# Kernel optimization log

Measured on AMD Instinct MI355X. Metric: run time of the kernel, lower is better.

## Reference

```python
import jax, jax.numpy as jnp
import numpy as np

N = 100000   # nodes
E = 1600000  # edges (avg degree 16)
D = 128      # in_features == out_features (required by residual branch)


def setup_inputs() -> dict:
    key = jax.random.key(0)
    ks = jax.random.split(key, 8)
    return {
        "x": jax.random.normal(ks[0], (N, D), dtype=jnp.float32),
        "W": jax.random.normal(ks[1], (D, D), dtype=jnp.float32) * (1.0 / np.sqrt(D)),
        "b": jax.random.normal(ks[2], (D,), dtype=jnp.float32) * 0.01,
        "Wres": jax.random.normal(ks[3], (D, D), dtype=jnp.float32) * (1.0 / np.sqrt(D)),
        "bres": jax.random.normal(ks[4], (D,), dtype=jnp.float32) * 0.01,
        "edge_val": jax.random.uniform(ks[5], (E,), dtype=jnp.float32),
        "edge_row": jax.random.randint(ks[6], (E,), 0, N, dtype=jnp.int32),
        "edge_col": jax.random.randint(ks[7], (E,), 0, N, dtype=jnp.int32),
    }


def reference(x, W, b, Wres, bres, edge_val, edge_row, edge_col):
    # Dense projection: [N, D]
    h = x @ W + b
    # Sparse adjacency SpMM: out[i] = sum_{e: row[e]==i} val[e] * h[col[e]]
    msgs = edge_val[:, None] * h[edge_col]            # [E, D] gather
    agg = jax.ops.segment_sum(msgs, edge_row, num_segments=N)  # [N, D] scatter-add
    # Activation (relu), then residual Linear applied to post-activation tensor
    # (faithful to the torch code: x = act(x); x = x + residual(x)).
    a = jax.nn.relu(agg)
    out = a + (a @ Wres + bres)
    # dropout = 0.0 -> identity (eval mode)
    return out
```

## Files before the change

### kernel.cpp

```cpp
#include <hip/hip_runtime.h>
#include <hip/hip_bf16.h>

#define D 128
#define RCH 128
#define NCH 782
#define NCHP 1024
#define NB_S 256
#define CH_S 6250
#define OS2 800
#define CAP 3072
#define GB 1563
#define PB 128

typedef __attribute__((ext_vector_type(8))) short short8v;
typedef __attribute__((ext_vector_type(4))) float float4v;

__device__ inline ushort f2bf(float f) {
    __hip_bfloat16 h = __float2bfloat16(f);
    return __builtin_bit_cast(ushort, h);
}
__device__ inline float bf2f(ushort u) {
    return __builtin_bit_cast(float, (uint)u << 16);
}
__device__ inline ushort relu_bf(ushort u) { return (u & 0x8000u) ? (ushort)0 : u; }

__device__ inline void stage_wt_lds(char* smem, const ushort* __restrict__ Wt,
                                    int tid) {
#pragma unroll
    for (int i = 0; i < 8; ++i) {
        const int L = tid * 128 + i * 16;
        const int row = L >> 8;
        const int off = L & 255;
        *(short8v*)(smem + row * 256 + (off ^ ((row & 7) << 4))) =
            *(const short8v*)((const char*)Wt + L);
    }
}

__global__ __launch_bounds__(256) void k1_prep(const float* __restrict__ W,
                                               const float* __restrict__ Wres,
                                               ushort* __restrict__ Wt,
                                               ushort* __restrict__ Wtres) {
    const int flat = blockIdx.x * 256 + threadIdx.x;
    const float* src = (flat < 16384) ? W : Wres;
    ushort* dst = (flat < 16384) ? Wt : Wtres;
    const int f = flat & 16383;
    const int k = f >> 7, c = f & 127;
    dst[c * D + k] = f2bf(src[f]);
}

__global__ __launch_bounds__(256) void k3_gemm0_p3(const float* __restrict__ X,
                                                   const ushort* __restrict__ Wt,
                                                   const float* __restrict__ bias,
                                                   ushort* __restrict__ hb, int N,
                                                   const float* __restrict__ ev,
                                                   const int* __restrict__ er,
                                                   const int* __restrict__ ec,
                                                   int* __restrict__ offs2,
                                                   int2* __restrict__ tmp, int E) {
    __shared__ char smem[32768];

    if (blockIdx.x < NB_S) {
        int* h = (int*)smem;
        int* sscan = (int*)(smem + 4 * NCHP);
        const int b = blockIdx.x;
        const int t = threadIdx.x;
        const int start = b * CH_S, end = min(E, start + CH_S);

        for (int k = t; k < NCHP; k += 256) h[k] = 0;
        __syncthreads();

        for (int e = start + t; e < end; e += 256)
            atomicAdd(&h[er[e] >> 7], 1);
        __syncthreads();

        const int a0 = h[4 * t], a1 = h[4 * t + 1];
        const int a2 = h[4 * t + 2], a3 = h[4 * t + 3];
        const int tsum = a0 + a1 + a2 + a3;
        sscan[t] = tsum;
        __syncthreads();
        for (int o = 1; o < 256; o <<= 1) {
            const int a = (t >= o) ? sscan[t - o] : 0;
            __syncthreads();
            sscan[t] += a;
            __syncthreads();
        }
        const int ex = b * CH_S + sscan[t] - tsum;
        const int c0 = 4 * t;
        h[c0]     = ex;
        h[c0 + 1] = ex + a0;
        h[c0 + 2] = ex + a0 + a1;
        h[c0 + 3] = ex + a0 + a1 + a2;
        int* od = offs2 + (long)b * OS2;
#pragma unroll
        for (int i = 0; i < 4; ++i)
            if (c0 + i <= NCH) od[c0 + i] = h[c0 + i];
        __syncthreads();

        for (int e = start + t; e < end; e += 256) {
            const int r = er[e];
            const int pos = atomicAdd(&h[r >> 7], 1);
            tmp[pos] = make_int2((ec[e] << 7) | (r & 127), __float_as_int(ev[e]));
        }
        return;
    }

    const int lane = threadIdx.x & 63;
    const int w = threadIdx.x >> 6;
    const int l16 = lane & 15;
    const int lk = lane >> 4;
    const long wRow = (long)(blockIdx.x - NB_S) * 64 + w * 16;

    short8v afrag[4];
    {
        long r = wRow + l16;
        if (r >= N) r = N - 1;
        const float* xp = X + r * D + lk * 8;
#pragma unroll
        for (int ks = 0; ks < 4; ++ks) {
            const float4 u0 = *(const float4*)(xp + ks * 32);
            const float4 u1 = *(const float4*)(xp + ks * 32 + 4);
            float f[8] = {u0.x, u0.y, u0.z, u0.w, u1.x, u1.y, u1.z, u1.w};
            short8v a;
#pragma unroll
            for (int i = 0; i < 8; ++i) a[i] = (short)f2bf(f[i]);
            afrag[ks] = a;
        }
    }

    stage_wt_lds(smem, Wt, threadIdx.x);
    __syncthreads();

    float4v acc[8];
#pragma unroll
    for (int t = 0; t < 8; ++t) acc[t] = (float4v)(0.0f);

    const int swz = (l16 & 7) << 4;
#pragma unroll
    for (int ks = 0; ks < 4; ++ks) {
#pragma unroll
        for (int t = 0; t < 8; ++t) {
            const int row = t * 16 + l16;
            const short8v bfrag = *(const short8v*)(
                smem + row * 256 + ((ks * 64 + lk * 16) ^ swz));
            acc[t] = __builtin_amdgcn_mfma_f32_16x16x32_bf16(afrag[ks], bfrag,
                                                             acc[t], 0, 0, 0);
        }
    }

#pragma unroll
    for (int t = 0; t < 8; ++t) {
        const int col = t * 16 + l16;
        const float bb = bias[col];
#pragma unroll
        for (int i = 0; i < 4; ++i) {
            const long row = wRow + lk * 4 + i;
            if (row < N) hb[row * D + col] = f2bf(acc[t][i] + bb);
        }
    }
}

__global__ __launch_bounds__(256) void k4_sort(const int2* __restrict__ tmp,
                                               const int* __restrict__ offs2,
                                               int2* __restrict__ recs,
                                               int* __restrict__ rowptr) {
    __shared__ int2 buf[CAP];
    __shared__ int sb[256];
    __shared__ int hcnt[RCH];
    __shared__ int sc[RCH];
    __shared__ int cur[RCH];
    const int c = blockIdx.x;
    const int t = threadIdx.x;
    const int s = c * CAP;

    const long ob = (long)t * OS2 + c;
    const int segs = offs2[ob];
    const int sege = offs2[ob + 1];
    const int cb = sege - segs;

    sb[t] = cb;
    __syncthreads();
    for (int o = 1; o < 256; o <<= 1) {
        const int a = (t >= o) ? sb[t - o] : 0;
        __syncthreads();
        sb[t] += a;
        __syncthreads();
    }
    const int base = sb[t] - cb;
    const int cnt = min(sb[255], CAP);

    if (t < RCH) hcnt[t] = 0;
    __syncthreads();

    for (int i = 0; i < cb; ++i) {
        const int p = base + i;
        if (p >= CAP) break;
        const int2 r = tmp[segs + i];
        buf[p] = r;
        atomicAdd(&hcnt[r.x & 127], 1);
    }
    __syncthreads();

    if (t < RCH) sc[t] = hcnt[t];
    __syncthreads();
    for (int o = 1; o < RCH; o <<= 1) {
        const int a = (t < RCH && t >= o) ? sc[t - o] : 0;
        __syncthreads();
        if (t < RCH) sc[t] += a;
        __syncthreads();
    }
    if (t < RCH) {
        const int ex = s + sc[t] - hcnt[t];
        cur[t] = ex;
        rowptr[c * (RCH + 1) + t] = ex;
    }
    if (t == 0) rowptr[c * (RCH + 1) + RCH] = s + cnt;
    __syncthreads();

    for (int k = t; k < cnt; k += 256) {
        const int2 r = buf[k];
        const int pos = atomicAdd(&cur[r.x & 127], 1);
        recs[pos] = make_int2((r.x >> 7) << 8, r.y);
    }
}

#define GFMA2(accv, rr, gg)                                                   \
    accv.x = fmaf(__int_as_float((rr).y), bf2f((ushort)((gg)&0xffffu)), accv.x);\
    accv.y = fmaf(__int_as_float((rr).y), bf2f((ushort)((gg) >> 16)), accv.y);

__device__ inline void drain_row(const int2* __restrict__ recs,
                                 const char* __restrict__ hpc,
                                 int& j, int e, float2& acc) {
    for (; j + 8 <= e; j += 8) {
        const int2 r0 = recs[j],     r1 = recs[j + 1];
        const int2 r2 = recs[j + 2], r3 = recs[j + 3];
        const int2 r4 = recs[j + 4], r5 = recs[j + 5];
        const int2 r6 = recs[j + 6], r7 = recs[j + 7];
        const uint g0 = *(const uint*)(hpc + (uint)r0.x);
        const uint g1 = *(const uint*)(hpc + (uint)r1.x);
        const uint g2 = *(const uint*)(hpc + (uint)r2.x);
        const uint g3 = *(const uint*)(hpc + (uint)r3.x);
        const uint g4 = *(const uint*)(hpc + (uint)r4.x);
        const uint g5 = *(const uint*)(hpc + (uint)r5.x);
        const uint g6 = *(const uint*)(hpc + (uint)r6.x);
        const uint g7 = *(const uint*)(hpc + (uint)r7.x);
        GFMA2(acc, r0, g0) GFMA2(acc, r1, g1) GFMA2(acc, r2, g2) GFMA2(acc, r3, g3)
        GFMA2(acc, r4, g4) GFMA2(acc, r5, g5) GFMA2(acc, r6, g6) GFMA2(acc, r7, g7)
    }
    for (; j + 2 <= e; j += 2) {
        const int2 r0 = recs[j], r1 = recs[j + 1];
        const uint g0 = *(const uint*)(hpc + (uint)r0.x);
        const uint g1 = *(const uint*)(hpc + (uint)r1.x);
        GFMA2(acc, r0, g0) GFMA2(acc, r1, g1)
    }
    if (j < e) {
        const int2 r0 = recs[j];
        const uint g0 = *(const uint*)(hpc + (uint)r0.x);
        GFMA2(acc, r0, g0)
    }
}

__global__ __launch_bounds__(256) void k5_spmm(const ushort* __restrict__ hb,
                                               const int2* __restrict__ recs,
                                               const int* __restrict__ rowptr,
                                               ushort* __restrict__ aggb, int N) {
    const int pair = blockIdx.x * 4 + (threadIdx.x >> 6);
    const int lane = threadIdx.x & 63;
    const int rowA = pair * 2;
    if (rowA >= N) return;

    const int c = rowA >> 7;
    const int tr = rowA & 127;
    int rp = 0;
    if (lane < 3) rp = rowptr[c * (RCH + 1) + tr + lane];
    const int sA = __shfl(rp, 0);
    const int eA = __shfl(rp, 1);
    const int sB = eA;
    const int eB = __shfl(rp, 2);

    const char* hpc = (const char*)hb + lane * 4;
    float2 accA = make_float2(0.f, 0.f);
    float2 accB = make_float2(0.f, 0.f);

    int jA = sA, jB = sB;
    while (jA + 8 <= eA && jB + 8 <= eB) {
        const int2 a0 = recs[jA],     a1 = recs[jA + 1];
        const int2 a2 = recs[jA + 2], a3 = recs[jA + 3];
        const int2 a4 = recs[jA + 4], a5 = recs[jA + 5];
        const int2 a6 = recs[jA + 6], a7 = recs[jA + 7];
        const int2 b0 = recs[jB],     b1 = recs[jB + 1];
        const int2 b2 = recs[jB + 2], b3 = recs[jB + 3];
        const int2 b4 = recs[jB + 4], b5 = recs[jB + 5];
        const int2 b6 = recs[jB + 6], b7 = recs[jB + 7];
        const uint ga0 = *(const uint*)(hpc + (uint)a0.x);
        const uint ga1 = *(const uint*)(hpc + (uint)a1.x);
        const uint ga2 = *(const uint*)(hpc + (uint)a2.x);
        const uint ga3 = *(const uint*)(hpc + (uint)a3.x);
        const uint ga4 = *(const uint*)(hpc + (uint)a4.x);
        const uint ga5 = *(const uint*)(hpc + (uint)a5.x);
        const uint ga6 = *(const uint*)(hpc + (uint)a6.x);
        const uint ga7 = *(const uint*)(hpc + (uint)a7.x);
        const uint gb0 = *(const uint*)(hpc + (uint)b0.x);
        const uint gb1 = *(const uint*)(hpc + (uint)b1.x);
        const uint gb2 = *(const uint*)(hpc + (uint)b2.x);
        const uint gb3 = *(const uint*)(hpc + (uint)b3.x);
        const uint gb4 = *(const uint*)(hpc + (uint)b4.x);
        const uint gb5 = *(const uint*)(hpc + (uint)b5.x);
        const uint gb6 = *(const uint*)(hpc + (uint)b6.x);
        const uint gb7 = *(const uint*)(hpc + (uint)b7.x);
        GFMA2(accA, a0, ga0) GFMA2(accA, a1, ga1) GFMA2(accA, a2, ga2) GFMA2(accA, a3, ga3)
        GFMA2(accA, a4, ga4) GFMA2(accA, a5, ga5) GFMA2(accA, a6, ga6) GFMA2(accA, a7, ga7)
        GFMA2(accB, b0, gb0) GFMA2(accB, b1, gb1) GFMA2(accB, b2, gb2) GFMA2(accB, b3, gb3)
        GFMA2(accB, b4, gb4) GFMA2(accB, b5, gb5) GFMA2(accB, b6, gb6) GFMA2(accB, b7, gb7)
        jA += 8;
        jB += 8;
    }
    drain_row(recs, hpc, jA, eA, accA);
    drain_row(recs, hpc, jB, eB, accB);

    const uint pA = (uint)f2bf(accA.x) | ((uint)f2bf(accA.y) << 16);
    *(uint*)(aggb + (long)rowA * D + lane * 2) = pA;
    const uint pB = (uint)f2bf(accB.x) | ((uint)f2bf(accB.y) << 16);
    *(uint*)(aggb + (long)(rowA + 1) * D + lane * 2) = pB;
}

__global__ __launch_bounds__(256) void k6_gemm1(const ushort* __restrict__ Xb,
                                                const ushort* __restrict__ Wt,
                                                const float* __restrict__ bias,
                                                float* __restrict__ Y, int N) {
    __shared__ char smem[32768];
    const int lane = threadIdx.x & 63;
    const int w = threadIdx.x >> 6;
    const int l16 = lane & 15;
    const int lk = lane >> 4;
    const long wRow = (long)blockIdx.x * 64 + w * 16;

    short8v afrag[4];
    {
        long r = wRow + l16;
        if (r >= N) r = N - 1;
        const ushort* xp = Xb + r * D + lk * 8;
#pragma unroll
        for (int ks = 0; ks < 4; ++ks) {
            short8v a = *(const short8v*)(xp + ks * 32);
#pragma unroll
            for (int i = 0; i < 8; ++i) a[i] = (short)relu_bf((ushort)a[i]);
            afrag[ks] = a;
        }
    }

    stage_wt_lds(smem, Wt, threadIdx.x);
    __syncthreads();

    float4v acc[8];
#pragma unroll
    for (int t = 0; t < 8; ++t) acc[t] = (float4v)(0.0f);

    const int swz = (l16 & 7) << 4;
#pragma unroll
    for (int ks = 0; ks < 4; ++ks) {
#pragma unroll
        for (int t = 0; t < 8; ++t) {
            const int row = t * 16 + l16;
            const short8v bfrag = *(const short8v*)(
                smem + row * 256 + ((ks * 64 + lk * 16) ^ swz));
            acc[t] = __builtin_amdgcn_mfma_f32_16x16x32_bf16(afrag[ks], bfrag,
                                                             acc[t], 0, 0, 0);
        }
    }

#pragma unroll
    for (int t = 0; t < 8; ++t) {
        const int col = t * 16 + l16;
        const float bb = bias[col];
#pragma unroll
        for (int i = 0; i < 4; ++i) {
            const long row = wRow + lk * 4 + i;
            if (row < N) {
                const float a = bf2f(relu_bf(Xb[row * D + col]));
                Y[row * D + col] = a + acc[t][i] + bb;
            }
        }
    }
}

extern "C" void kernel_launch(void* const* d_in, const int* in_sizes, int n_in,
                              void* d_out, int out_size, void* d_ws, size_t ws_size,
                              hipStream_t stream) {
    const float* x    = (const float*)d_in[0];
    const float* W    = (const float*)d_in[1];
    const float* b    = (const float*)d_in[2];
    const float* Wres = (const float*)d_in[3];
    const float* bres = (const float*)d_in[4];
    const float* ev   = (const float*)d_in[5];
    const int*   er   = (const int*)d_in[6];
    const int*   ec   = (const int*)d_in[7];

    float* out = (float*)d_out;

    const int n = in_sizes[0] / D;
    const int e = in_sizes[5];

    char* ws = (char*)d_ws;
    size_t off_b = 0;
    auto alloc = [&](size_t bytes) {
        void* p = ws + off_b;
        off_b += (bytes + 511) & ~size_t(511);
        return p;
    };
    ushort* hb     = (ushort*)alloc((size_t)n * D * sizeof(ushort));
    int2*   recs   = (int2*)alloc((size_t)NCH * CAP * sizeof(int2));
    int*    rowptr = (int*)alloc((size_t)NCH * (RCH + 1) * sizeof(int));
    ushort* Wt     = (ushort*)alloc((size_t)D * D * sizeof(ushort));
    ushort* Wtres  = (ushort*)alloc((size_t)D * D * sizeof(ushort));
    const size_t overlay = off_b;
    int2*   tmp    = (int2*)alloc((size_t)NB_S * CH_S * sizeof(int2));
    int*    offs2  = (int*)alloc((size_t)NB_S * OS2 * sizeof(int));
    size_t aggb_end = overlay + (size_t)n * D * sizeof(ushort);
    if (aggb_end > off_b) off_b = aggb_end;
    ushort* aggb = (ushort*)(ws + overlay);
    (void)ws_size;

    k1_prep<<<PB, 256, 0, stream>>>(W, Wres, Wt, Wtres);

    k3_gemm0_p3<<<NB_S + GB, 256, 0, stream>>>(x, Wt, b, hb, n,
                                               ev, er, ec, offs2, tmp, e);

    k4_sort<<<NCH, 256, 0, stream>>>(tmp, offs2, recs, rowptr);

    k5_spmm<<<(n / 2 + 3) / 4, 256, 0, stream>>>(hb, recs, rowptr, aggb, n);

    k6_gemm1<<<(n + 63) / 64, 256, 0, stream>>>(aggb, Wtres, bres, out, n);
}
```

Before: 162.1 us.

## Split scatter and GEMM into separate kernels with more scatter blocks

Separates the fused edge-bucketing and first-GEMM kernel into two launches. The scatter kernel now uses 500 blocks of 3200 edges, reads edge arrays with int4/float4 vector loads, and the sort kernel has each thread merge two segments. The GEMM kernel processes 128 rows per block, so each staged weight tile is reused twice. This aims to balance the long scatter blocks against GEMM blocks and cut per-edge load overhead, at the cost of an extra launch and losing overlap between the two phases.

Result: no change. 162.4 us (+0.2%).

```diff
diff --git a/kernel.cpp b/kernel.cpp
--- a/kernel.cpp
+++ b/kernel.cpp
@@ -5,11 +5,10 @@
 #define RCH 128
 #define NCH 782
 #define NCHP 1024
-#define NB_S 256
-#define CH_S 6250
+#define NB_S 500
+#define CH_S 3200
 #define OS2 800
 #define CAP 3072
-#define GB 1563
 #define PB 128
 
 typedef __attribute__((ext_vector_type(8))) short short8v;
@@ -48,113 +47,138 @@
     dst[c * D + k] = f2bf(src[f]);
 }
 
-__global__ __launch_bounds__(256) void k3_gemm0_p3(const float* __restrict__ X,
-                                                   const ushort* __restrict__ Wt,
-                                                   const float* __restrict__ bias,
-                                                   ushort* __restrict__ hb, int N,
-                                                   const float* __restrict__ ev,
+__global__ __launch_bounds__(256) void k3a_scatter(const float* __restrict__ ev,
                                                    const int* __restrict__ er,
                                                    const int* __restrict__ ec,
                                                    int* __restrict__ offs2,
                                                    int2* __restrict__ tmp, int E) {
+    __shared__ int h[NCHP];
+    __shared__ int sscan[256];
+    const int b = blockIdx.x;
+    const int t = threadIdx.x;
+    const int start = b * CH_S;
+    const int end = min(E, start + CH_S);
+    const int nfull = (end - start) & ~3;
+
+    for (int k = t; k < NCHP; k += 256) h[k] = 0;
+    __syncthreads();
+
+    for (int o = 4 * t; o < nfull; o += 1024) {
+        const int4 r4 = *(const int4*)(er + start + o);
+        atomicAdd(&h[r4.x >> 7], 1);
+        atomicAdd(&h[r4.y >> 7], 1);
+        atomicAdd(&h[r4.z >> 7], 1);
+        atomicAdd(&h[r4.w >> 7], 1);
+    }
+    for (int o = nfull + t; o < end - start; o += 256)
+        atomicAdd(&h[er[start + o] >> 7], 1);
+    __syncthreads();
+
+    const int a0 = h[4 * t], a1 = h[4 * t + 1];
+    const int a2 = h[4 * t + 2], a3 = h[4 * t + 3];
+    const int tsum = a0 + a1 + a2 + a3;
+    sscan[t] = tsum;
+    __syncthreads();
+    for (int o = 1; o < 256; o <<= 1) {
+        const int a = (t >= o) ? sscan[t - o] : 0;
+        __syncthreads();
+        sscan[t] += a;
+        __syncthreads();
+    }
+    const int ex = start + sscan[t] - tsum;
+    const int c0 = 4 * t;
+    h[c0]     = ex;
+    h[c0 + 1] = ex + a0;
+    h[c0 + 2] = ex + a0 + a1;
+    h[c0 + 3] = ex + a0 + a1 + a2;
+    int* od = offs2 + (long)b * OS2;
+#pragma unroll
+    for (int i = 0; i < 4; ++i)
+        if (c0 + i <= NCH) od[c0 + i] = h[c0 + i];
+    __syncthreads();
+
+    for (int o = 4 * t; o < nfull; o += 1024) {
+        const int4 r4 = *(const int4*)(er + start + o);
+        const int4 c4 = *(const int4*)(ec + start + o);
+        const float4 v4 = *(const float4*)(ev + start + o);
+        const int p0 = atomicAdd(&h[r4.x >> 7], 1);
+        const int p1 = atomicAdd(&h[r4.y >> 7], 1);
+        const int p2 = atomicAdd(&h[r4.z >> 7], 1);
+        const int p3 = atomicAdd(&h[r4.w >> 7], 1);
+        tmp[p0] = make_int2((c4.x << 7) | (r4.x & 127), __float_as_int(v4.x));
+        tmp[p1] = make_int2((c4.y << 7) | (r4.y & 127), __float_as_int(v4.y));
+        tmp[p2] = make_int2((c4.z << 7) | (r4.z & 127), __float_as_int(v4.z));
+        tmp[p3] = make_int2((c4.w << 7) | (r4.w & 127), __float_as_int(v4.w));
+    }
+    for (int o = nfull + t; o < end - start; o += 256) {
+        const int e = start + o;
+        const int r = er[e];
+        const int pos = atomicAdd(&h[r >> 7], 1);
+        tmp[pos] = make_int2((ec[e] << 7) | (r & 127), __float_as_int(ev[e]));
+    }
+}
+
+__global__ __launch_bounds__(256) void k3b_gemm0(const float* __restrict__ X,
+                                                 const ushort* __restrict__ Wt,
+                                                 const float* __restrict__ bias,
+                                                 ushort* __restrict__ hb, int N) {
     __shared__ char smem[32768];
-
-    if (blockIdx.x < NB_S) {
-        int* h = (int*)smem;
-        int* sscan = (int*)(smem + 4 * NCHP);
-        const int b = blockIdx.x;
-        const int t = threadIdx.x;
-        const int start = b * CH_S, end = min(E, start + CH_S);
-
-        for (int k = t; k < NCHP; k += 256) h[k] = 0;
-        __syncthreads();
-
-        for (int e = start + t; e < end; e += 256)
-            atomicAdd(&h[er[e] >> 7], 1);
-        __syncthreads();
-
-        const int a0 = h[4 * t], a1 = h[4 * t + 1];
-        const int a2 = h[4 * t + 2], a3 = h[4 * t + 3];
-        const int tsum = a0 + a1 + a2 + a3;
-        sscan[t] = tsum;
-        __syncthreads();
-        for (int o = 1; o < 256; o <<= 1) {
-            const int a = (t >= o) ? sscan[t - o] : 0;
-            __syncthreads();
-            sscan[t] += a;
-            __syncthreads();
-        }
-        const int ex = b * CH_S + sscan[t] - tsum;
-        const int c0 = 4 * t;
-        h[c0]     = ex;
-        h[c0 + 1] = ex + a0;
-        h[c0 + 2] = ex + a0 + a1;
-        h[c0 + 3] = ex + a0 + a1 + a2;
-        int* od = offs2 + (long)b * OS2;
-#pragma unroll
-        for (int i = 0; i < 4; ++i)
-            if (c0 + i <= NCH) od[c0 + i] = h[c0 + i];
-        __syncthreads();
-
-        for (int e = start + t; e < end; e += 256) {
-            const int r = er[e];
-            const int pos = atomicAdd(&h[r >> 7], 1);
-            tmp[pos] = make_int2((ec[e] << 7) | (r & 127), __float_as_int(ev[e]));
-        }
-        return;
-    }
-
     const int lane = threadIdx.x & 63;
     const int w = threadIdx.x >> 6;
     const int l16 = lane & 15;
     const int lk = lane >> 4;
-    const long wRow = (long)(blockIdx.x - NB_S) * 64 + w * 16;
-
-    short8v afrag[4];
-    {
-        long r = wRow + l16;
-        if (r >= N) r = N - 1;
-        const float* xp = X + r * D + lk * 8;
+
+    stage_wt_lds(smem, Wt, threadIdx.x);
+    __syncthreads();
+
+    const int swz = (l16 & 7) << 4;
+
+#pragma unroll
+    for (int j = 0; j < 2; ++j) {
+        const long wRow = (long)blockIdx.x * 128 + j * 64 + w * 16;
+
+        short8v afrag[4];
+        {
+            long r = wRow + l16;
+            if (r >= N) r = N - 1;
+            const float* xp = X + r * D + lk * 8;
+#pragma unroll
+            for (int ks = 0; ks < 4; ++ks) {
+                const float4 u0 = *(const float4*)(xp + ks * 32);
+                const float4 u1 = *(const float4*)(xp + ks * 32 + 4);
+                float f[8] = {u0.x, u0.y, u0.z, u0.w, u1.x, u1.y, u1.z, u1.w};
+                short8v a;
+#pragma unroll
+                for (int i = 0; i < 8; ++i) a[i] = (short)f2bf(f[i]);
+                afrag[ks] = a;
+            }
+        }
+
+        float4v acc[8];
+#pragma unroll
+        for (int t = 0; t < 8; ++t) acc[t] = (float4v)(0.0f);
+
 #pragma unroll
         for (int ks = 0; ks < 4; ++ks) {
-            const float4 u0 = *(const float4*)(xp + ks * 32);
-            const float4 u1 = *(const float4*)(xp + ks * 32 + 4);
-            float f[8] = {u0.x, u0.y, u0.z, u0.w, u1.x, u1.y, u1.z, u1.w};
-            short8v a;
-#pragma unroll
-            for (int i = 0; i < 8; ++i) a[i] = (short)f2bf(f[i]);
-            afrag[ks] = a;
-        }
-    }
-
-    stage_wt_lds(smem, Wt, threadIdx.x);
-    __syncthreads();
-
-    float4v acc[8];
-#pragma unroll
-    for (int t = 0; t < 8; ++t) acc[t] = (float4v)(0.0f);
-
-    const int swz = (l16 & 7) << 4;
-#pragma unroll
-    for (int ks = 0; ks < 4; ++ks) {
+#pragma unroll
+            for (int t = 0; t < 8; ++t) {
+                const int row = t * 16 + l16;
+                const short8v bfrag = *(const short8v*)(
+                    smem + row * 256 + ((ks * 64 + lk * 16) ^ swz));
+                acc[t] = __builtin_amdgcn_mfma_f32_16x16x32_bf16(afrag[ks], bfrag,
+                                                                 acc[t], 0, 0, 0);
+            }
+        }
+
 #pragma unroll
         for (int t = 0; t < 8; ++t) {
-            const int row = t * 16 + l16;
-            const short8v bfrag = *(const short8v*)(
-                smem + row * 256 + ((ks * 64 + lk * 16) ^ swz));
-            acc[t] = __builtin_amdgcn_mfma_f32_16x16x32_bf16(afrag[ks], bfrag,
-                                                             acc[t], 0, 0, 0);
-        }
-    }
-
-#pragma unroll
-    for (int t = 0; t < 8; ++t) {
-        const int col = t * 16 + l16;
-        const float bb = bias[col];
-#pragma unroll
-        for (int i = 0; i < 4; ++i) {
-            const long row = wRow + lk * 4 + i;
-            if (row < N) hb[row * D + col] = f2bf(acc[t][i] + bb);
+            const int col = t * 16 + l16;
+            const float bb = bias[col];
+#pragma unroll
+            for (int i = 0; i < 4; ++i) {
+                const long row = wRow + lk * 4 + i;
+                if (row < N) hb[row * D + col] = f2bf(acc[t][i] + bb);
+            }
         }
     }
 }
@@ -172,10 +196,14 @@
     const int t = threadIdx.x;
     const int s = c * CAP;
 
-    const long ob = (long)t * OS2 + c;
-    const int segs = offs2[ob];
-    const int sege = offs2[ob + 1];
-    const int cb = sege - segs;
+    int segA = 0, cbA = 0, segB = 0, cbB = 0;
+    if (t < NB_S / 2) {
+        const int* oA = offs2 + (long)(2 * t) * OS2;
+        const int* oB = offs2 + (long)(2 * t + 1) * OS2;
+        segA = oA[c]; cbA = oA[c + 1] - segA;
+        segB = oB[c]; cbB = oB[c + 1] - segB;
+    }
+    const int cb = cbA + cbB;
 
     sb[t] = cb;
     __syncthreads();
@@ -191,10 +219,17 @@
     if (t < RCH) hcnt[t] = 0;
     __syncthreads();
 
-    for (int i = 0; i < cb; ++i) {
+    for (int i = 0; i < cbA; ++i) {
         const int p = base + i;
         if (p >= CAP) break;
-        const int2 r = tmp[segs + i];
+        const int2 r = tmp[segA + i];
+        buf[p] = r;
+        atomicAdd(&hcnt[r.x & 127], 1);
+    }
+    for (int i = 0; i < cbB; ++i) {
+        const int p = base + cbA + i;
+        if (p >= CAP) break;
+        const int2 r = tmp[segB + i];
         buf[p] = r;
         atomicAdd(&hcnt[r.x & 127], 1);
     }
@@ -422,8 +457,9 @@
 
     k1_prep<<<PB, 256, 0, stream>>>(W, Wres, Wt, Wtres);
 
-    k3_gemm0_p3<<<NB_S + GB, 256, 0, stream>>>(x, Wt, b, hb, n,
-                                               ev, er, ec, offs2, tmp, e);
+    k3a_scatter<<<NB_S, 256, 0, stream>>>(ev, er, ec, offs2, tmp, e);
+
+    k3b_gemm0<<<(n + 127) / 128, 256, 0, stream>>>(x, Wt, b, hb, n);
 
     k4_sort<<<NCH, 256, 0, stream>>>(tmp, offs2, recs, rowptr);
 
```
